# Optimization experiments

Measured on AMD Instinct MI355X. Metric: run time of the kernel, lower is better.

Reference implementation:

```python
import jax, jax.numpy as jnp
import numpy as np

DIM = 1024
NUM_HEADS = 16
HEAD_DIM = DIM // NUM_HEADS
SCALE = HEAD_DIM ** -0.5


def setup_inputs() -> dict:
    key = jax.random.key(0)
    ks = jax.random.split(key, 8)
    B, N, L = 2, 256, 8192
    x = jax.random.normal(ks[0], (B, N, DIM), dtype=jnp.float32)
    past_k = jax.random.normal(ks[1], (B, NUM_HEADS, L, HEAD_DIM), dtype=jnp.float32)
    past_v = jax.random.normal(ks[2], (B, NUM_HEADS, L, HEAD_DIM), dtype=jnp.float32)
    s = DIM ** -0.5
    w_qkv = jax.random.normal(ks[3], (DIM, 3 * DIM), dtype=jnp.float32) * s
    b_qkv = jnp.zeros((3 * DIM,), dtype=jnp.float32)
    w_proj = jax.random.normal(ks[4], (DIM, DIM), dtype=jnp.float32) * s
    b_proj = jnp.zeros((DIM,), dtype=jnp.float32)
    return {"x": x, "past_k": past_k, "past_v": past_v,
            "w_qkv": w_qkv, "b_qkv": b_qkv, "w_proj": w_proj, "b_proj": b_proj}


def reference(x, past_k, past_v, w_qkv, b_qkv, w_proj, b_proj):
    B, N, C = x.shape
    qkv = (x @ w_qkv + b_qkv).reshape(B, N, 3, NUM_HEADS, HEAD_DIM)
    qkv = jnp.transpose(qkv, (2, 0, 3, 1, 4))
    q, k_new, v_new = qkv[0], qkv[1], qkv[2]
    # Streaming KV cache append (torch.cat along seq dim)
    k_all = jnp.concatenate([past_k, k_new], axis=-2)  # [B, H, L+N, D]
    v_all = jnp.concatenate([past_v, v_new], axis=-2)
    # Scaled dot-product attention (non-causal full attention over cache)
    scores = jnp.einsum("bhnd,bhld->bhnl", q, k_all) * SCALE
    attn = jax.nn.softmax(scores, axis=-1)
    out = jnp.einsum("bhnl,bhld->bhnd", attn, v_all)  # [B, H, N, D]
    out = jnp.transpose(out, (0, 2, 1, 3)).reshape(B, N, C)
    return out @ w_proj + b_proj
```

## Files before the change

kernel.cpp:

```cpp
#include <hip/hip_runtime.h>
#include <hip/hip_bf16.h>


#define BB 2
#define NH 16
#define NQ 256
#define HD 64
#define DIMC 1024
#define LPAST 8192
#define TOTK 8448
#define NSPLIT 16

typedef __attribute__((ext_vector_type(8))) short short8;
typedef __attribute__((ext_vector_type(4))) float f32x4;
typedef __attribute__((ext_vector_type(4))) int int4v;

#define DEVI static __device__ __forceinline__

DEVI float exp2g(float x) { return __builtin_amdgcn_exp2f(x); }

DEVI int cvtpk(float lo, float hi) {
  int r;
  asm("v_cvt_pk_bf16_f32 %0, %1, %2" : "=v"(r) : "v"(lo), "v"(hi));
  return r;
}
DEVI short f2bf(float f) {
  union { float f; unsigned u; } v; v.f = f;
  unsigned r = v.u + 0x7FFFu + ((v.u >> 16) & 1u);
  return (short)(r >> 16);
}

template<int MODE>
__global__ __launch_bounds__(256, 2) void gemm_k(
    const float* __restrict__ A, const float* __restrict__ Bm,
    const float* __restrict__ bias, float* __restrict__ Cout,
    short* __restrict__ qbuf, float* __restrict__ knew, float* __restrict__ vnew,
    int M, int Nn, int K)
{
  __shared__ alignas(16) short As[64][72];
  __shared__ alignas(16) short Bs[64][72];
  const int tid = threadIdx.x;
  const int lane = tid & 63, wave = tid >> 6;
  const int nblk = Nn >> 6;
  const int bi = blockIdx.x / nblk, bj = blockIdx.x % nblk;
  const int wm = wave >> 1, wn = wave & 1;
  const int g = lane >> 4, l16 = lane & 15;
  f32x4 acc[2][2] = {};
  const int r = tid >> 2, q4 = (tid & 3) << 4;

  for (int k0 = 0; k0 < K; k0 += 64) {
    const float* pa = A + (size_t)(bi * 64 + r) * K + (k0 + q4);
    float4 a0 = ((const float4*)pa)[0];
    float4 a1 = ((const float4*)pa)[1];
    float4 a2 = ((const float4*)pa)[2];
    float4 a3 = ((const float4*)pa)[3];
    const float* pb = Bm + (size_t)(k0 + r) * Nn + (bj * 64 + q4);
    float4 b0 = ((const float4*)pb)[0];
    float4 b1 = ((const float4*)pb)[1];
    float4 b2 = ((const float4*)pb)[2];
    float4 b3 = ((const float4*)pb)[3];
    __syncthreads();
    {
      int4v p0 = {cvtpk(a0.x,a0.y), cvtpk(a0.z,a0.w), cvtpk(a1.x,a1.y), cvtpk(a1.z,a1.w)};
      int4v p1 = {cvtpk(a2.x,a2.y), cvtpk(a2.z,a2.w), cvtpk(a3.x,a3.y), cvtpk(a3.z,a3.w)};
      *(int4v*)&As[r][q4]     = p0;
      *(int4v*)&As[r][q4 + 8] = p1;
    }
    Bs[q4+ 0][r] = f2bf(b0.x); Bs[q4+ 1][r] = f2bf(b0.y);
    Bs[q4+ 2][r] = f2bf(b0.z); Bs[q4+ 3][r] = f2bf(b0.w);
    Bs[q4+ 4][r] = f2bf(b1.x); Bs[q4+ 5][r] = f2bf(b1.y);
    Bs[q4+ 6][r] = f2bf(b1.z); Bs[q4+ 7][r] = f2bf(b1.w);
    Bs[q4+ 8][r] = f2bf(b2.x); Bs[q4+ 9][r] = f2bf(b2.y);
    Bs[q4+10][r] = f2bf(b2.z); Bs[q4+11][r] = f2bf(b2.w);
    Bs[q4+12][r] = f2bf(b3.x); Bs[q4+13][r] = f2bf(b3.y);
    Bs[q4+14][r] = f2bf(b3.z); Bs[q4+15][r] = f2bf(b3.w);
    __syncthreads();
    #pragma unroll
    for (int kf = 0; kf < 2; ++kf) {
      short8 af[2], bfv[2];
      #pragma unroll
      for (int mt = 0; mt < 2; ++mt)
        af[mt] = *(const short8*)&As[wm*32 + mt*16 + l16][kf*32 + g*8];
      #pragma unroll
      for (int nt = 0; nt < 2; ++nt)
        bfv[nt] = *(const short8*)&Bs[wn*32 + nt*16 + l16][kf*32 + g*8];
      #pragma unroll
      for (int mt = 0; mt < 2; ++mt)
        #pragma unroll
        for (int nt = 0; nt < 2; ++nt)
          acc[mt][nt] = __builtin_amdgcn_mfma_f32_16x16x32_bf16(
              af[mt], bfv[nt], acc[mt][nt], 0, 0, 0);
    }
  }

  #pragma unroll
  for (int mt = 0; mt < 2; ++mt)
    #pragma unroll
    for (int nt = 0; nt < 2; ++nt)
      #pragma unroll
      for (int rg = 0; rg < 4; ++rg) {
        int row = bi*64 + wm*32 + mt*16 + g*4 + rg;
        int col = bj*64 + wn*32 + nt*16 + l16;
        float val = acc[mt][nt][rg] + bias[col];
        if (MODE == 0) {
          Cout[(size_t)row * Nn + col] = val;
        } else {
          int which = col >> 10, cc = col & 1023;
          int h = cc >> 6, d = cc & 63;
          int b = row >> 8, n = row & 255;
          size_t idx = (((size_t)(b*NH + h))*NQ + n)*HD + d;
          if (which == 0)      qbuf[idx] = f2bf(val * 0.180336878f);
          else if (which == 1) knew[idx] = val;
          else                 vnew[idx] = val;
        }
      }
}

__global__ __launch_bounds__(512, 2) void attn_k(
    const short* __restrict__ qbuf, const float* __restrict__ pastk,
    const float* __restrict__ pastv, const float* __restrict__ knew,
    const float* __restrict__ vnew, float* __restrict__ opart,
    float* __restrict__ mbuf, float* __restrict__ lbuf)
{
  __shared__ alignas(16) short Kt[2][64][72];
  __shared__ alignas(16) short Vt[2][64][70];
  const int tid = threadIdx.x;
  const int lane = tid & 63, wave = tid >> 6;
  const int g = lane >> 4, l16 = lane & 15;
  const int s = blockIdx.x & (NSPLIT - 1), bh = blockIdx.x / NSPLIT;
  const int kr = tid >> 3, q8 = (tid & 7) << 3;
  const int vp = tid >> 4, d4 = (tid & 15) << 2;

  short8 qf[2][2];
  #pragma unroll
  for (int qt = 0; qt < 2; ++qt)
    #pragma unroll
    for (int half = 0; half < 2; ++half)
      qf[qt][half] = *(const short8*)(qbuf +
          ((size_t)bh*NQ + wave*32 + qt*16 + l16)*HD + half*32 + g*8);

  f32x4 acc[2][4] = {};
  float m_s[2], l_s[2];
  #pragma unroll
  for (int qt = 0; qt < 2; ++qt) { m_s[qt] = -INFINITY; l_s[qt] = 0.f; }

  const int first  = 8*s + (s < 4 ? s : 4);
  const int nsteps = 8 + (s < 4 ? 1 : 0);

  float4 ka[2], va, vc;
  auto load = [&](int step) {
    const float* kp = (step < 128)
        ? pastk + ((size_t)bh*LPAST + step*64 + kr)*HD + q8
        : knew  + ((size_t)bh*NQ + (step - 128)*64 + kr)*HD + q8;
    ka[0] = ((const float4*)kp)[0];
    ka[1] = ((const float4*)kp)[1];
    const float* vq = (step < 128)
        ? pastv + ((size_t)bh*LPAST + step*64 + 2*vp)*HD + d4
        : vnew  + ((size_t)bh*NQ + (step - 128)*64 + 2*vp)*HD + d4;
    va = *(const float4*)vq;
    vc = *(const float4*)(vq + HD);
  };
  auto stage = [&](int b) {
    const float* kf32 = (const float*)ka;
    int4v p = {cvtpk(kf32[0],kf32[1]), cvtpk(kf32[2],kf32[3]),
               cvtpk(kf32[4],kf32[5]), cvtpk(kf32[6],kf32[7])};
    *(int4v*)&Kt[b][kr][q8] = p;
    const float* af = (const float*)&va;
    const float* cf = (const float*)&vc;
    #pragma unroll
    for (int j = 0; j < 4; ++j)
      *(int*)&Vt[b][d4 + j][2*vp] = cvtpk(af[j], cf[j]);
  };

  load(first);
  stage(0);
  if (nsteps > 1) load(first + 1);
  __syncthreads();

  for (int it = 0; it < nsteps; ++it) {
    const int cur = it & 1;

    short8 pa[2][2];
    #pragma unroll
    for (int qt = 0; qt < 2; ++qt) {
      f32x4 sv[4];
      #pragma unroll
      for (int kt = 0; kt < 4; ++kt) {
        short8 k0 = *(const short8*)&Kt[cur][kt*16 + l16][g*8];
        short8 k1 = *(const short8*)&Kt[cur][kt*16 + l16][32 + g*8];
        f32x4 z = {0.f, 0.f, 0.f, 0.f};
        z = __builtin_amdgcn_mfma_f32_16x16x32_bf16(k0, qf[qt][0], z, 0,0,0);
        sv[kt] = __builtin_amdgcn_mfma_f32_16x16x32_bf16(k1, qf[qt][1], z, 0,0,0);
      }
      float mx = sv[0][0];
      #pragma unroll
      for (int kt = 0; kt < 4; ++kt)
        #pragma unroll
        for (int rg = 0; rg < 4; ++rg) mx = fmaxf(mx, sv[kt][rg]);
      mx = fmaxf(mx, __shfl_xor(mx, 16));
      mx = fmaxf(mx, __shfl_xor(mx, 32));
      float m_new = fmaxf(m_s[qt], mx);
      float al = exp2g(m_s[qt] - m_new);
      float ss = 0.f;
      #pragma unroll
      for (int kt = 0; kt < 4; ++kt)
        #pragma unroll
        for (int rg = 0; rg < 4; ++rg) {
          float p = exp2g(sv[kt][rg] - m_new);
          sv[kt][rg] = p; ss += p;
        }
      ss += __shfl_xor(ss, 16);
      ss += __shfl_xor(ss, 32);
      l_s[qt] = l_s[qt]*al + ss;
      m_s[qt] = m_new;
      #pragma unroll
      for (int rg = 0; rg < 4; ++rg) {
        float a = __shfl(al, g*4 + rg);
        #pragma unroll
        for (int dt = 0; dt < 4; ++dt) acc[qt][dt][rg] *= a;
      }
      int4v w0 = {cvtpk(sv[0][0],sv[0][1]), cvtpk(sv[0][2],sv[0][3]),
                  cvtpk(sv[1][0],sv[1][1]), cvtpk(sv[1][2],sv[1][3])};
      int4v w1 = {cvtpk(sv[2][0],sv[2][1]), cvtpk(sv[2][2],sv[2][3]),
                  cvtpk(sv[3][0],sv[3][1]), cvtpk(sv[3][2],sv[3][3])};
      pa[qt][0] = __builtin_bit_cast(short8, w0);
      pa[qt][1] = __builtin_bit_cast(short8, w1);
    }

    #pragma unroll
    for (int kk = 0; kk < 2; ++kk) {
      #pragma unroll
      for (int dt = 0; dt < 4; ++dt) {
        const short* vrow = &Vt[cur][dt*16 + l16][kk*32 + 4*g];
        int i0 = *(const int*)(vrow);
        int i1 = *(const int*)(vrow + 2);
        int i2 = *(const int*)(vrow + 16);
        int i3 = *(const int*)(vrow + 18);
        int4v iv = {i0, i1, i2, i3};
        short8 vf = __builtin_bit_cast(short8, iv);
        #pragma unroll
        for (int qt = 0; qt < 2; ++qt)
          acc[qt][dt] = __builtin_amdgcn_mfma_f32_16x16x32_bf16(
              pa[qt][kk], vf, acc[qt][dt], 0,0,0);
      }
    }

    if (it + 1 < nsteps) {
      stage(1 - cur);
      if (it + 2 < nsteps) load(first + it + 2);
      __syncthreads();
    }
  }

  size_t pbase = ((size_t)(bh * NSPLIT + s)) * NQ;
  #pragma unroll
  for (int qt = 0; qt < 2; ++qt)
    #pragma unroll
    for (int dt = 0; dt < 4; ++dt)
      #pragma unroll
      for (int rg = 0; rg < 4; ++rg) {
        int row = wave*32 + qt*16 + g*4 + rg;
        int col = dt*16 + l16;
        opart[(pbase + row)*HD + col] = acc[qt][dt][rg];
      }
  if (g == 0) {
    #pragma unroll
    for (int qt = 0; qt < 2; ++qt) {
      int q = wave*32 + qt*16 + l16;
      mbuf[pbase + q] = m_s[qt];
      lbuf[pbase + q] = l_s[qt];
    }
  }
}

__global__ __launch_bounds__(256) void combine_k(
    const float* __restrict__ opart, const float* __restrict__ mbuf,
    const float* __restrict__ lbuf, float* __restrict__ attnout)
{
  const int lane = threadIdx.x & 63, wave = threadIdx.x >> 6;
  const int rid = blockIdx.x * 4 + wave;
  const int bh = rid >> 8, n = rid & 255;
  const int b = bh >> 4, h = bh & 15;
  float M = -INFINITY;
  float ms[NSPLIT], ls[NSPLIT];
  #pragma unroll
  for (int s = 0; s < NSPLIT; ++s) {
    size_t base = ((size_t)(bh * NSPLIT + s)) * NQ + n;
    ms[s] = mbuf[base]; ls[s] = lbuf[base];
    M = fmaxf(M, ms[s]);
  }
  float denom = 0.f, o = 0.f;
  #pragma unroll
  for (int s = 0; s < NSPLIT; ++s) {
    float w = exp2g(ms[s] - M);
    denom += w * ls[s];
    o += w * opart[(((size_t)(bh * NSPLIT + s)) * NQ + n) * HD + lane];
  }
  attnout[((size_t)(b * NQ + n)) * DIMC + h * HD + lane] = o / denom;
}

extern "C" void kernel_launch(void* const* d_in, const int* in_sizes, int n_in,
                              void* d_out, int out_size, void* d_ws, size_t ws_size,
                              hipStream_t stream)
{
  const float* x     = (const float*)d_in[0];
  const float* pastk = (const float*)d_in[1];
  const float* pastv = (const float*)d_in[2];
  const float* wqkv  = (const float*)d_in[3];
  const float* bqkv  = (const float*)d_in[4];
  const float* wproj = (const float*)d_in[5];
  const float* bproj = (const float*)d_in[6];
  float* out = (float*)d_out;
  char* ws = (char*)d_ws;

  size_t off = 0;
  short* qbuf   = (short*)(ws + off); off += (size_t)BB*NH*NQ*HD*2;
  float* knew   = (float*)(ws + off); off += (size_t)BB*NH*NQ*HD*4;
  float* vnew   = (float*)(ws + off); off += (size_t)BB*NH*NQ*HD*4;
  float* opart  = (float*)(ws + off); off += (size_t)BB*NH*NSPLIT*NQ*HD*4;
  float* mbuf   = (float*)(ws + off); off += (size_t)BB*NH*NSPLIT*NQ*4;
  float* lbuf   = (float*)(ws + off); off += (size_t)BB*NH*NSPLIT*NQ*4;
  float* attnout= (float*)(ws + off); off += (size_t)BB*NQ*DIMC*4;

  gemm_k<1><<<(512/64)*(3072/64), 256, 0, stream>>>(
      x, wqkv, bqkv, nullptr, qbuf, knew, vnew, 512, 3072, 1024);
  attn_k<<<BB*NH*NSPLIT, 512, 0, stream>>>(
      qbuf, pastk, pastv, knew, vnew, opart, mbuf, lbuf);
  combine_k<<<BB*NH*NQ/4, 256, 0, stream>>>(opart, mbuf, lbuf, attnout);
  gemm_k<0><<<(512/64)*(1024/64), 256, 0, stream>>>(
      attnout, wproj, bproj, out, nullptr, nullptr, nullptr, 512, 1024, 1024);
}
```

Measured before the change: 91.82 us.

## Switch attention kernel to 32x32x16 MFMA with swizzled LDS and lazy rescale

Rewrites the attention inner loop to use 32x32x16 bf16 MFMA tiles, so each wave handles 32 queries as one tile instead of two 16-row tiles. K/V shared tiles drop their padding and use XOR swizzles to avoid bank conflicts, with a permuted V staging layout to match the new fragment order. The online softmax skips rescaling the accumulator unless the running max grows by more than 8 (in log2 units), and s_setprio is raised around the MFMA blocks. Risks include more register pressure from 16-wide accumulators and scalar V loads from global memory.

```diff
diff --git a/kernel.cpp b/kernel.cpp
--- a/kernel.cpp
+++ b/kernel.cpp
@@ -13,6 +13,7 @@
 
 typedef __attribute__((ext_vector_type(8))) short short8;
 typedef __attribute__((ext_vector_type(4))) float f32x4;
+typedef __attribute__((ext_vector_type(16))) float f32x16;
 typedef __attribute__((ext_vector_type(4))) int int4v;
 
 #define DEVI static __device__ __forceinline__
@@ -122,54 +123,50 @@
     const float* __restrict__ vnew, float* __restrict__ opart,
     float* __restrict__ mbuf, float* __restrict__ lbuf)
 {
-  __shared__ alignas(16) short Kt[2][64][72];
-  __shared__ alignas(16) short Vt[2][64][70];
+  __shared__ alignas(16) short Kt[2][64][64];
+  __shared__ alignas(16) short Vt[2][64][64];
   const int tid = threadIdx.x;
   const int lane = tid & 63, wave = tid >> 6;
-  const int g = lane >> 4, l16 = lane & 15;
+  const int h = lane >> 5, c = lane & 31;
   const int s = blockIdx.x & (NSPLIT - 1), bh = blockIdx.x / NSPLIT;
-  const int kr = tid >> 3, q8 = (tid & 7) << 3;
-  const int vp = tid >> 4, d4 = (tid & 15) << 2;
-
-  short8 qf[2][2];
-  #pragma unroll
-  for (int qt = 0; qt < 2; ++qt)
-    #pragma unroll
-    for (int half = 0; half < 2; ++half)
-      qf[qt][half] = *(const short8*)(qbuf +
-          ((size_t)bh*NQ + wave*32 + qt*16 + l16)*HD + half*32 + g*8);
-
-  f32x4 acc[2][4] = {};
-  float m_s[2], l_s[2];
-  #pragma unroll
-  for (int qt = 0; qt < 2; ++qt) { m_s[qt] = -INFINITY; l_s[qt] = 0.f; }
+  const int kr = tid >> 3, kc8 = (tid & 7) << 3;
+  const int vp = tid >> 4, vd = tid & 15;
+  const int vpi = ((vp>>4)<<5) | (((vp>>2)&1)<<4) | (((vp>>1)&1)<<3)
+                | (((vp>>3)&1)<<2) | ((vp&1)<<1);
+  const int vsw = vpi ^ ((vd & 7) << 3);
+  const int csw = (c & 7) << 3;
+
+  short8 qf[4];
+  #pragma unroll
+  for (int dk = 0; dk < 4; ++dk)
+    qf[dk] = *(const short8*)(qbuf + ((size_t)bh*NQ + wave*32 + c)*HD + 16*dk + 8*h);
+
+  f32x16 acc[2] = {};
+  float m_s = -INFINITY, l_s = 0.f;
 
   const int first  = 8*s + (s < 4 ? s : 4);
   const int nsteps = 8 + (s < 4 ? 1 : 0);
 
-  float4 ka[2], va, vc;
+  float kfl[8], vlo[4], vhi[4];
   auto load = [&](int step) {
     const float* kp = (step < 128)
-        ? pastk + ((size_t)bh*LPAST + step*64 + kr)*HD + q8
-        : knew  + ((size_t)bh*NQ + (step - 128)*64 + kr)*HD + q8;
-    ka[0] = ((const float4*)kp)[0];
-    ka[1] = ((const float4*)kp)[1];
+        ? pastk + ((size_t)bh*LPAST + step*64 + kr)*HD + kc8
+        : knew  + ((size_t)bh*NQ + (step - 128)*64 + kr)*HD + kc8;
+    *(float4*)&kfl[0] = *(const float4*)kp;
+    *(float4*)&kfl[4] = *(const float4*)(kp + 4);
     const float* vq = (step < 128)
-        ? pastv + ((size_t)bh*LPAST + step*64 + 2*vp)*HD + d4
-        : vnew  + ((size_t)bh*NQ + (step - 128)*64 + 2*vp)*HD + d4;
-    va = *(const float4*)vq;
-    vc = *(const float4*)(vq + HD);
+        ? pastv + ((size_t)bh*LPAST + step*64 + 2*vp)*HD + vd
+        : vnew  + ((size_t)bh*NQ + (step - 128)*64 + 2*vp)*HD + vd;
+    #pragma unroll
+    for (int j = 0; j < 4; ++j) { vlo[j] = vq[16*j]; vhi[j] = vq[HD + 16*j]; }
   };
   auto stage = [&](int b) {
-    const float* kf32 = (const float*)ka;
-    int4v p = {cvtpk(kf32[0],kf32[1]), cvtpk(kf32[2],kf32[3]),
-               cvtpk(kf32[4],kf32[5]), cvtpk(kf32[6],kf32[7])};
-    *(int4v*)&Kt[b][kr][q8] = p;
-    const float* af = (const float*)&va;
-    const float* cf = (const float*)&vc;
+    int4v kp4 = {cvtpk(kfl[0],kfl[1]), cvtpk(kfl[2],kfl[3]),
+                 cvtpk(kfl[4],kfl[5]), cvtpk(kfl[6],kfl[7])};
+    *(int4v*)&Kt[b][kr][kc8 ^ ((kr & 7) << 3)] = kp4;
     #pragma unroll
     for (int j = 0; j < 4; ++j)
-      *(int*)&Vt[b][d4 + j][2*vp] = cvtpk(af[j], cf[j]);
+      *(int*)&Vt[b][vd + 16*j][vsw] = cvtpk(vlo[j], vhi[j]);
   };
 
   load(first);
@@ -180,70 +177,73 @@
   for (int it = 0; it < nsteps; ++it) {
     const int cur = it & 1;
 
-    short8 pa[2][2];
-    #pragma unroll
-    for (int qt = 0; qt < 2; ++qt) {
-      f32x4 sv[4];
-      #pragma unroll
-      for (int kt = 0; kt < 4; ++kt) {
-        short8 k0 = *(const short8*)&Kt[cur][kt*16 + l16][g*8];
-        short8 k1 = *(const short8*)&Kt[cur][kt*16 + l16][32 + g*8];
-        f32x4 z = {0.f, 0.f, 0.f, 0.f};
-        z = __builtin_amdgcn_mfma_f32_16x16x32_bf16(k0, qf[qt][0], z, 0,0,0);
-        sv[kt] = __builtin_amdgcn_mfma_f32_16x16x32_bf16(k1, qf[qt][1], z, 0,0,0);
+    f32x16 sv0 = {}, sv1 = {};
+    __builtin_amdgcn_s_setprio(1);
+    #pragma unroll
+    for (int dk = 0; dk < 4; ++dk) {
+      short8 k0 = *(const short8*)&Kt[cur][c][(16*dk + 8*h) ^ csw];
+      sv0 = __builtin_amdgcn_mfma_f32_32x32x16_bf16(k0, qf[dk], sv0, 0,0,0);
+    }
+    #pragma unroll
+    for (int dk = 0; dk < 4; ++dk) {
+      short8 k1 = *(const short8*)&Kt[cur][32 + c][(16*dk + 8*h) ^ csw];
+      sv1 = __builtin_amdgcn_mfma_f32_32x32x16_bf16(k1, qf[dk], sv1, 0,0,0);
+    }
+    __builtin_amdgcn_s_setprio(0);
+
+    float t16[16];
+    #pragma unroll
+    for (int r = 0; r < 16; ++r) t16[r] = fmaxf(sv0[r], sv1[r]);
+    #pragma unroll
+    for (int w = 8; w >= 1; w >>= 1)
+      #pragma unroll
+      for (int r = 0; r < w; ++r) t16[r] = fmaxf(t16[r], t16[r + w]);
+    float mx = fmaxf(t16[0], __shfl_xor(t16[0], 32));
+
+    if (!__all(mx <= m_s + 8.f)) {
+      float mn = fmaxf(m_s, mx);
+      float al = exp2g(m_s - mn);
+      l_s *= al;
+      #pragma unroll
+      for (int r = 0; r < 16; ++r) {
+        float a = __shfl(al, (r&3) + 8*(r>>2) + 4*h);
+        acc[0][r] *= a; acc[1][r] *= a;
       }
-      float mx = sv[0][0];
-      #pragma unroll
-      for (int kt = 0; kt < 4; ++kt)
-        #pragma unroll
-        for (int rg = 0; rg < 4; ++rg) mx = fmaxf(mx, sv[kt][rg]);
-      mx = fmaxf(mx, __shfl_xor(mx, 16));
-      mx = fmaxf(mx, __shfl_xor(mx, 32));
-      float m_new = fmaxf(m_s[qt], mx);
-      float al = exp2g(m_s[qt] - m_new);
-      float ss = 0.f;
-      #pragma unroll
-      for (int kt = 0; kt < 4; ++kt)
-        #pragma unroll
-        for (int rg = 0; rg < 4; ++rg) {
-          float p = exp2g(sv[kt][rg] - m_new);
-          sv[kt][rg] = p; ss += p;
-        }
-      ss += __shfl_xor(ss, 16);
-      ss += __shfl_xor(ss, 32);
-      l_s[qt] = l_s[qt]*al + ss;
-      m_s[qt] = m_new;
-      #pragma unroll
-      for (int rg = 0; rg < 4; ++rg) {
-        float a = __shfl(al, g*4 + rg);
-        #pragma unroll
-        for (int dt = 0; dt < 4; ++dt) acc[qt][dt][rg] *= a;
+      m_s = mn;
+    }
+    float ss = 0.f;
+    #pragma unroll
+    for (int r = 0; r < 16; ++r) {
+      float p0 = exp2g(sv0[r] - m_s); sv0[r] = p0;
+      float p1 = exp2g(sv1[r] - m_s); sv1[r] = p1;
+      ss += p0 + p1;
+    }
+    ss += __shfl_xor(ss, 32);
+    l_s += ss;
+
+    short8 pa[4];
+    #pragma unroll
+    for (int kc = 0; kc < 4; ++kc) {
+      int4v w;
+      #pragma unroll
+      for (int jd = 0; jd < 4; ++jd) {
+        int r0 = 8*(jd>>1) + 4*(kc&1) + 2*(jd&1);
+        w[jd] = (kc < 2) ? cvtpk(sv0[r0], sv0[r0+1])
+                         : cvtpk(sv1[r0], sv1[r0+1]);
       }
-      int4v w0 = {cvtpk(sv[0][0],sv[0][1]), cvtpk(sv[0][2],sv[0][3]),
-                  cvtpk(sv[1][0],sv[1][1]), cvtpk(sv[1][2],sv[1][3])};
-      int4v w1 = {cvtpk(sv[2][0],sv[2][1]), cvtpk(sv[2][2],sv[2][3]),
-                  cvtpk(sv[3][0],sv[3][1]), cvtpk(sv[3][2],sv[3][3])};
-      pa[qt][0] = __builtin_bit_cast(short8, w0);
-      pa[qt][1] = __builtin_bit_cast(short8, w1);
-    }
-
-    #pragma unroll
-    for (int kk = 0; kk < 2; ++kk) {
-      #pragma unroll
-      for (int dt = 0; dt < 4; ++dt) {
-        const short* vrow = &Vt[cur][dt*16 + l16][kk*32 + 4*g];
-        int i0 = *(const int*)(vrow);
-        int i1 = *(const int*)(vrow + 2);
-        int i2 = *(const int*)(vrow + 16);
-        int i3 = *(const int*)(vrow + 18);
-        int4v iv = {i0, i1, i2, i3};
-        short8 vf = __builtin_bit_cast(short8, iv);
-        #pragma unroll
-        for (int qt = 0; qt < 2; ++qt)
-          acc[qt][dt] = __builtin_amdgcn_mfma_f32_16x16x32_bf16(
-              pa[qt][kk], vf, acc[qt][dt], 0,0,0);
+      pa[kc] = __builtin_bit_cast(short8, w);
+    }
+
+    __builtin_amdgcn_s_setprio(1);
+    #pragma unroll
+    for (int kc = 0; kc < 4; ++kc) {
+      #pragma unroll
+      for (int dt = 0; dt < 2; ++dt) {
+        short8 vf = *(const short8*)&Vt[cur][32*dt + c][(16*kc + 8*h) ^ csw];
+        acc[dt] = __builtin_amdgcn_mfma_f32_32x32x16_bf16(pa[kc], vf, acc[dt], 0,0,0);
       }
     }
+    __builtin_amdgcn_s_setprio(0);
 
     if (it + 1 < nsteps) {
       stage(1 - cur);
@@ -254,22 +254,15 @@
 
   size_t pbase = ((size_t)(bh * NSPLIT + s)) * NQ;
   #pragma unroll
-  for (int qt = 0; qt < 2; ++qt)
-    #pragma unroll
-    for (int dt = 0; dt < 4; ++dt)
-      #pragma unroll
-      for (int rg = 0; rg < 4; ++rg) {
-        int row = wave*32 + qt*16 + g*4 + rg;
-        int col = dt*16 + l16;
-        opart[(pbase + row)*HD + col] = acc[qt][dt][rg];
-      }
-  if (g == 0) {
-    #pragma unroll
-    for (int qt = 0; qt < 2; ++qt) {
-      int q = wave*32 + qt*16 + l16;
-      mbuf[pbase + q] = m_s[qt];
-      lbuf[pbase + q] = l_s[qt];
-    }
+  for (int dt = 0; dt < 2; ++dt)
+    #pragma unroll
+    for (int r = 0; r < 16; ++r) {
+      int row = wave*32 + (r&3) + 8*(r>>2) + 4*h;
+      opart[(pbase + row)*HD + 32*dt + c] = acc[dt][r];
+    }
+  if (lane < 32) {
+    mbuf[pbase + wave*32 + c] = m_s;
+    lbuf[pbase + wave*32 + c] = l_s;
   }
 }
 
```

Result: faster. 89.39 us (-2.6%).
